# Performance work log

Measured on AMD Instinct MI355X. Metric: run time of the kernel, lower is better.

## Reference

```python
import jax, jax.numpy as jnp
import numpy as np

B, D_IN, D_H = 8192, 512, 1024


def setup_inputs() -> dict:
    key = jax.random.key(0)
    ks = jax.random.split(key, 5)
    # Kaiming-normal-ish init: std = sqrt(2/fan_in)
    Wx = jax.random.normal(ks[0], (D_IN, 4 * D_H), jnp.float32) * np.sqrt(2.0 / D_IN)
    Wh = jax.random.normal(ks[1], (D_H, 4 * D_H), jnp.float32) * np.sqrt(2.0 / D_H)
    b = jnp.zeros((4 * D_H,), jnp.float32)
    x = jax.random.normal(ks[2], (B, D_IN), jnp.float32)
    h = jax.random.normal(ks[3], (B, D_H), jnp.float32)
    c = jax.random.normal(ks[4], (B, D_H), jnp.float32)
    return {"x": x, "h": h, "c": c, "Wx": Wx, "Wh": Wh, "b": b}


def reference(x, h, c, Wx, Wh, b):
    # Fused gate pre-activations: [B, 4H] in gate order (g, i, f, o)
    gates = x @ Wx + h @ Wh + b[None, :]
    g_in, i_in, f_in, o_in = jnp.split(gates, 4, axis=-1)
    g_out = jnp.tanh(g_in)
    i_out = jax.nn.sigmoid(i_in)
    # NOTE: faithful to the original source's bug — f_out and o_out both use i_in.
    f_out = jax.nn.sigmoid(i_in)
    o_out = jax.nn.sigmoid(i_in)
    c_new = g_out * i_out + f_out * c
    h_new = jnp.tanh(c_new) * o_out
    return h_new, c_new
```

## Files before the change

kernel.cpp:

```cpp
#include <hip/hip_runtime.h>
#include <hip/hip_bf16.h>
#include <cstdint>

#define BROWS 8192
#define DIN   512
#define DH    1024
#define KTOT  1536
#define NT    (KTOT / 64)

typedef __bf16 bf16x8 __attribute__((ext_vector_type(8)));
typedef __bf16 bf16x4 __attribute__((ext_vector_type(4)));
typedef float  f32x4  __attribute__((ext_vector_type(4)));

__device__ __forceinline__ void load16_to_lds(const void* gptr, void* lptr) {
    __builtin_amdgcn_global_load_lds(
        (const __attribute__((address_space(1))) uint32_t*)gptr,
        (__attribute__((address_space(3))) uint32_t*)lptr,
        16, 0, 0);
}

__global__ __launch_bounds__(256) void cvtA_kernel(
    const float* __restrict__ x, const float* __restrict__ h,
    __bf16* __restrict__ A) {
    int t = blockIdx.x * 256 + threadIdx.x;
    int row = t / 192;
    int j = t - row * 192;
    int kg = j * 8;
    const float* src = (kg < DIN) ? (x + (size_t)row * DIN + kg)
                                  : (h + (size_t)row * DH + (kg - DIN));
    float4 u = *(const float4*)src;
    float4 v = *(const float4*)(src + 4);
    bf16x8 o = { (__bf16)u.x, (__bf16)u.y, (__bf16)u.z, (__bf16)u.w,
                 (__bf16)v.x, (__bf16)v.y, (__bf16)v.z, (__bf16)v.w };
    int swz = (j * 16) ^ ((row & 7) << 4);
    *(bf16x8*)((char*)A + (size_t)row * 3072 + swz) = o;
}

__global__ __launch_bounds__(256) void cvtB_kernel(
    const float* __restrict__ Wx, const float* __restrict__ Wh,
    __bf16* __restrict__ Bt) {
    __shared__ float tile[32][33];
    int k0 = blockIdx.x * 32;
    int n0 = blockIdx.y * 32;
    int tx = threadIdx.x;
    int ty = threadIdx.y;
#pragma unroll
    for (int i = 0; i < 4; ++i) {
        int k = k0 + ty + 8 * i;
        float v = (k < DIN) ? Wx[(size_t)k * 4096 + n0 + tx]
                            : Wh[(size_t)(k - DIN) * 4096 + n0 + tx];
        tile[ty + 8 * i][tx] = v;
    }
    __syncthreads();
    int n = n0 + tx;
    int kk = ty * 4;
    bf16x4 o = { (__bf16)tile[kk][tx], (__bf16)tile[kk + 1][tx],
                 (__bf16)tile[kk + 2][tx], (__bf16)tile[kk + 3][tx] };
    int swz = ((k0 + kk) * 2) ^ ((n & 7) << 4);
    *(bf16x4*)((char*)Bt + (size_t)n * 3072 + swz) = o;
}


#define BARRIER  do { __builtin_amdgcn_sched_barrier(0); __builtin_amdgcn_s_barrier(); __builtin_amdgcn_sched_barrier(0); } while (0)
#define VMW(n)   do { asm volatile("s_waitcnt vmcnt(" #n ")" ::: "memory"); __builtin_amdgcn_sched_barrier(0); } while (0)
#define LGKM0    do { asm volatile("s_waitcnt lgkmcnt(0)" ::: "memory"); __builtin_amdgcn_sched_barrier(0); } while (0)

#define STAGE_A(buf, kt) do {                                                  \
    const char* g0_ = Ab + (size_t)(brow + r0) * 3072                          \
                         + (size_t)(kt) * 128 + cb;                            \
    char* l0_ = sAb + (buf) * 16384 + r0 * 128 + cb;                           \
    load16_to_lds(g0_, l0_);                                                   \
    load16_to_lds(g0_ + 64 * 3072, l0_ + 64 * 128);                            \
} while (0)

#define STAGE_BG(buf, kt) do {                                                 \
    const char* g0_ = Bb + (size_t)(bnp + r0) * 3072                           \
                         + (size_t)(kt) * 128 + cb;                            \
    load16_to_lds(g0_, sBb + (buf) * 16384 + r0 * 128 + cb);                   \
} while (0)

#define STAGE_BI(buf, kt) do {                                                 \
    const char* g0_ = Bb + (size_t)(1024 + bnp + r0) * 3072                    \
                         + (size_t)(kt) * 128 + cb;                            \
    load16_to_lds(g0_, sBb + (buf) * 16384 + (64 + r0) * 128 + cb);            \
} while (0)

#define READ_A(dst, c)                                                         \
    _Pragma("unroll")                                                          \
    for (int m2_ = 0; m2_ < 2; ++m2_) {                                        \
        _Pragma("unroll")                                                      \
        for (int ks_ = 0; ks_ < 2; ++ks_) {                                    \
            int row_ = wrow + m2_ * 16 + l15;                                  \
            int kb_ = ks_ * 64 + l4x16;                                        \
            dst[m2_][ks_] = *(const bf16x8*)(sAb + (c) * 16384 + row_ * 128    \
                                             + (kb_ ^ swzkey));                \
        }                                                                      \
    }

#define READ_BG(dst, c)                                                        \
    _Pragma("unroll")                                                          \
    for (int ni_ = 0; ni_ < 2; ++ni_) {                                        \
        _Pragma("unroll")                                                      \
        for (int ks_ = 0; ks_ < 2; ++ks_) {                                    \
            int row_ = wcol + ni_ * 16 + l15;                                  \
            int kb_ = ks_ * 64 + l4x16;                                        \
            dst[ni_][ks_] = *(const bf16x8*)(sBb + (c) * 16384 + row_ * 128    \
                                             + (kb_ ^ swzkey));                \
        }                                                                      \
    }

#define READ_BI(dst, c)                                                        \
    _Pragma("unroll")                                                          \
    for (int ni_ = 0; ni_ < 2; ++ni_) {                                        \
        _Pragma("unroll")                                                      \
        for (int ks_ = 0; ks_ < 2; ++ks_) {                                    \
            int row_ = 64 + wcol + ni_ * 16 + l15;                             \
            int kb_ = ks_ * 64 + l4x16;                                        \
            dst[ni_][ks_] = *(const bf16x8*)(sBb + (c) * 16384 + row_ * 128    \
                                             + (kb_ ^ swzkey));                \
        }                                                                      \
    }

#define MMA(ACC, AF, BF) do {                                                  \
    __builtin_amdgcn_s_setprio(1);                                             \
    _Pragma("unroll")                                                          \
    for (int ks_ = 0; ks_ < 2; ++ks_) {                                        \
        _Pragma("unroll")                                                      \
        for (int m2_ = 0; m2_ < 2; ++m2_) {                                    \
            _Pragma("unroll")                                                  \
            for (int ni_ = 0; ni_ < 2; ++ni_) {                                \
                ACC[m2_][ni_] = __builtin_amdgcn_mfma_f32_16x16x32_bf16(       \
                    AF[m2_][ks_], BF[ni_][ks_], ACC[m2_][ni_], 0, 0, 0);       \
            }                                                                  \
        }                                                                      \
    }                                                                          \
    __builtin_amdgcn_s_setprio(0);                                             \
    __builtin_amdgcn_sched_barrier(0);                                         \
} while (0)

__global__ __launch_bounds__(512, 4) void lstm_gemm_kernel(
    const __bf16* __restrict__ A,
    const __bf16* __restrict__ Bt,
    const float* __restrict__ bias,
    const float* __restrict__ c_in,
    float* __restrict__ out_h,
    float* __restrict__ out_c) {
    __shared__ __bf16 sA[2][128][64];
    __shared__ __bf16 sB[2][128][64];

    const int tid  = threadIdx.x;
    const int lane = tid & 63;
    const int wid  = tid >> 6;
    const int wr   = wid & 3;
    const int wc   = wid >> 2;

    const int bid   = blockIdx.x;
    const int xcd   = bid & 7;
    const int idx   = bid >> 3;
    const int band  = xcd * 8 + (idx & 7);
    const int panel = idx >> 3;
    const int brow  = band * 128;
    const int bnp   = panel * 64;

    const int l15    = lane & 15;
    const int l4x16  = (lane >> 4) * 16;
    const int swzkey = (l15 & 7) << 4;
    const int wrow   = wr * 32;
    const int wcol   = wc * 32;

    const int r0 = tid >> 3;
    const int cb = (tid & 7) * 16;

    const char* Ab = (const char*)A;
    const char* Bb = (const char*)Bt;
    char* sAb = (char*)&sA[0][0][0];
    char* sBb = (char*)&sB[0][0][0];

    f32x4 accg[2][2], acci[2][2];
#pragma unroll
    for (int mi = 0; mi < 2; ++mi)
#pragma unroll
        for (int ni = 0; ni < 2; ++ni) {
            accg[mi][ni] = (f32x4){0.f, 0.f, 0.f, 0.f};
            acci[mi][ni] = (f32x4){0.f, 0.f, 0.f, 0.f};
        }

    bf16x8 aF[2][2], bgF[2][2], biF[2][2];

    STAGE_A(0, 0);
    STAGE_BG(0, 0);
    STAGE_BI(0, 0);

    for (int t = 0; t < NT - 1; ++t) {
        const int c  = t & 1;
        const int nb = c ^ 1;
        VMW(1); BARRIER;
        READ_A(aF, c);
        READ_BG(bgF, c);
        STAGE_A(nb, t + 1);
        BARRIER; LGKM0;
        MMA(accg, aF, bgF);
        VMW(2); BARRIER;
        READ_BI(biF, c);
        STAGE_BG(nb, t + 1);
        STAGE_BI(nb, t + 1);
        BARRIER; LGKM0;
        MMA(acci, aF, biF);
    }
    {
        const int c = (NT - 1) & 1;
        VMW(1); BARRIER;
        READ_A(aF, c);
        READ_BG(bgF, c);
        BARRIER; LGKM0;
        MMA(accg, aF, bgF);
        VMW(0); BARRIER;
        READ_BI(biF, c);
        BARRIER; LGKM0;
        MMA(acci, aF, biF);
    }

    const int R0 = brow + wrow;
    const int C0 = bnp + wcol;
    const int l4 = lane >> 4;
#pragma unroll
    for (int ni = 0; ni < 2; ++ni) {
        const int col = C0 + ni * 16 + l15;
        const float bg = bias[col];
        const float bi = bias[1024 + col];
#pragma unroll
        for (int mi = 0; mi < 2; ++mi) {
#pragma unroll
            for (int r = 0; r < 4; ++r) {
                const int row = R0 + mi * 16 + l4 * 4 + r;
                const float g_in = accg[mi][ni][r] + bg;
                const float i_in = acci[mi][ni][r] + bi;
                const float s  = 1.0f / (1.0f + __expf(-i_in));
                const float tg = 2.0f / (1.0f + __expf(-2.0f * g_in)) - 1.0f;
                const float cv = c_in[(size_t)row * DH + col];
                const float cn = s * (tg + cv);
                const float hn = (2.0f / (1.0f + __expf(-2.0f * cn)) - 1.0f) * s;
                out_h[(size_t)row * DH + col] = hn;
                out_c[(size_t)row * DH + col] = cn;
            }
        }
    }
}

extern "C" void kernel_launch(void* const* d_in, const int* in_sizes, int n_in,
                              void* d_out, int out_size, void* d_ws, size_t ws_size,
                              hipStream_t stream) {
    const float* x  = (const float*)d_in[0];
    const float* h  = (const float*)d_in[1];
    const float* c  = (const float*)d_in[2];
    const float* Wx = (const float*)d_in[3];
    const float* Wh = (const float*)d_in[4];
    const float* b  = (const float*)d_in[5];

    __bf16* A  = (__bf16*)d_ws;
    __bf16* Bt = (__bf16*)((char*)d_ws + (size_t)BROWS * KTOT * 2);

    float* out_h = (float*)d_out;
    float* out_c = out_h + (size_t)BROWS * DH;

    cvtA_kernel<<<(BROWS * (KTOT / 8)) / 256, 256, 0, stream>>>(x, h, A);
    cvtB_kernel<<<dim3(KTOT / 32, 2048 / 32), dim3(32, 8), 0, stream>>>(Wx, Wh, Bt);
    lstm_gemm_kernel<<<1024, 512, 0, stream>>>(A, Bt, b, c, out_h, out_c);
}
```

Before: 84.37 us.

## Load B fragments directly from global memory, keeping only A staged in LDS

The weight (B) operand no longer goes through LDS. Each wave reads its B fragments straight from global memory in an unswizzled layout, while only the A tile is double-buffered in shared memory. Blocks shrink to 4 waves, each covering 64 rows, with a new block-to-tile mapping and fewer barriers. This cuts LDS traffic and synchronisation, but exposes global-memory latency on B and leans on L2 reuse of the weights across blocks.

```diff
diff --git a/kernel.cpp b/kernel.cpp
--- a/kernel.cpp
+++ b/kernel.cpp
@@ -56,8 +56,7 @@
     int kk = ty * 4;
     bf16x4 o = { (__bf16)tile[kk][tx], (__bf16)tile[kk + 1][tx],
                  (__bf16)tile[kk + 2][tx], (__bf16)tile[kk + 3][tx] };
-    int swz = ((k0 + kk) * 2) ^ ((n & 7) << 4);
-    *(bf16x4*)((char*)Bt + (size_t)n * 3072 + swz) = o;
+    *(bf16x4*)(Bt + (size_t)n * KTOT + k0 + kk) = o;
 }
 
 
@@ -66,71 +65,50 @@
 #define LGKM0    do { asm volatile("s_waitcnt lgkmcnt(0)" ::: "memory"); __builtin_amdgcn_sched_barrier(0); } while (0)
 
 #define STAGE_A(buf, kt) do {                                                  \
-    const char* g0_ = Ab + (size_t)(brow + r0) * 3072                          \
-                         + (size_t)(kt) * 128 + cb;                            \
-    char* l0_ = sAb + (buf) * 16384 + r0 * 128 + cb;                           \
-    load16_to_lds(g0_, l0_);                                                   \
-    load16_to_lds(g0_ + 64 * 3072, l0_ + 64 * 128);                            \
+    _Pragma("unroll")                                                          \
+    for (int p_ = 0; p_ < 4; ++p_) {                                           \
+        const char* g_ = Ab + (size_t)(brow + p_ * 32 + r0) * 3072             \
+                            + (size_t)(kt) * 128 + cb;                         \
+        load16_to_lds(g_, sAb + (buf) * 16384 + (p_ * 32 + r0) * 128 + cb);    \
+    }                                                                          \
+    __builtin_amdgcn_sched_barrier(0);                                         \
 } while (0)
 
-#define STAGE_BG(buf, kt) do {                                                 \
-    const char* g0_ = Bb + (size_t)(bnp + r0) * 3072                           \
-                         + (size_t)(kt) * 128 + cb;                            \
-    load16_to_lds(g0_, sBb + (buf) * 16384 + r0 * 128 + cb);                   \
-} while (0)
-
-#define STAGE_BI(buf, kt) do {                                                 \
-    const char* g0_ = Bb + (size_t)(1024 + bnp + r0) * 3072                    \
-                         + (size_t)(kt) * 128 + cb;                            \
-    load16_to_lds(g0_, sBb + (buf) * 16384 + (64 + r0) * 128 + cb);            \
-} while (0)
-
-#define READ_A(dst, c)                                                         \
-    _Pragma("unroll")                                                          \
-    for (int m2_ = 0; m2_ < 2; ++m2_) {                                        \
+#define READ_A(c)                                                              \
+    _Pragma("unroll")                                                          \
+    for (int m_ = 0; m_ < 4; ++m_) {                                           \
         _Pragma("unroll")                                                      \
         for (int ks_ = 0; ks_ < 2; ++ks_) {                                    \
-            int row_ = wrow + m2_ * 16 + l15;                                  \
+            int row_ = wrow + m_ * 16 + l15;                                   \
             int kb_ = ks_ * 64 + l4x16;                                        \
-            dst[m2_][ks_] = *(const bf16x8*)(sAb + (c) * 16384 + row_ * 128    \
-                                             + (kb_ ^ swzkey));                \
+            aF[m_][ks_] = *(const bf16x8*)(sAb + (c) * 16384 + row_ * 128      \
+                                           + (kb_ ^ swzkey));                  \
         }                                                                      \
     }
 
-#define READ_BG(dst, c)                                                        \
+#define LOAD_B(dst, rowbase, kt) do {                                          \
     _Pragma("unroll")                                                          \
     for (int ni_ = 0; ni_ < 2; ++ni_) {                                        \
         _Pragma("unroll")                                                      \
         for (int ks_ = 0; ks_ < 2; ++ks_) {                                    \
-            int row_ = wcol + ni_ * 16 + l15;                                  \
-            int kb_ = ks_ * 64 + l4x16;                                        \
-            dst[ni_][ks_] = *(const bf16x8*)(sBb + (c) * 16384 + row_ * 128    \
-                                             + (kb_ ^ swzkey));                \
+            dst[ni_][ks_] = *(const bf16x8*)(Bt                                \
+                + (size_t)((rowbase) + ni_ * 16) * KTOT                        \
+                + (kt) * 64 + ks_ * 32 + l4x8);                                \
         }                                                                      \
-    }
-
-#define READ_BI(dst, c)                                                        \
-    _Pragma("unroll")                                                          \
-    for (int ni_ = 0; ni_ < 2; ++ni_) {                                        \
-        _Pragma("unroll")                                                      \
-        for (int ks_ = 0; ks_ < 2; ++ks_) {                                    \
-            int row_ = 64 + wcol + ni_ * 16 + l15;                             \
-            int kb_ = ks_ * 64 + l4x16;                                        \
-            dst[ni_][ks_] = *(const bf16x8*)(sBb + (c) * 16384 + row_ * 128    \
-                                             + (kb_ ^ swzkey));                \
-        }                                                                      \
-    }
+    }                                                                          \
+    __builtin_amdgcn_sched_barrier(0);                                         \
+} while (0)
 
 #define MMA(ACC, AF, BF) do {                                                  \
     __builtin_amdgcn_s_setprio(1);                                             \
     _Pragma("unroll")                                                          \
     for (int ks_ = 0; ks_ < 2; ++ks_) {                                        \
         _Pragma("unroll")                                                      \
-        for (int m2_ = 0; m2_ < 2; ++m2_) {                                    \
+        for (int m_ = 0; m_ < 4; ++m_) {                                       \
             _Pragma("unroll")                                                  \
             for (int ni_ = 0; ni_ < 2; ++ni_) {                                \
-                ACC[m2_][ni_] = __builtin_amdgcn_mfma_f32_16x16x32_bf16(       \
-                    AF[m2_][ks_], BF[ni_][ks_], ACC[m2_][ni_], 0, 0, 0);       \
+                ACC[m_][ni_] = __builtin_amdgcn_mfma_f32_16x16x32_bf16(        \
+                    AF[m_][ks_], BF[ni_][ks_], ACC[m_][ni_], 0, 0, 0);         \
             }                                                                  \
         }                                                                      \
     }                                                                          \
@@ -138,7 +116,7 @@
     __builtin_amdgcn_sched_barrier(0);                                         \
 } while (0)
 
-__global__ __launch_bounds__(512, 4) void lstm_gemm_kernel(
+__global__ __launch_bounds__(256, 3) void lstm_gemm_kernel(
     const __bf16* __restrict__ A,
     const __bf16* __restrict__ Bt,
     const float* __restrict__ bias,
@@ -146,82 +124,80 @@
     float* __restrict__ out_h,
     float* __restrict__ out_c) {
     __shared__ __bf16 sA[2][128][64];
-    __shared__ __bf16 sB[2][128][64];
 
     const int tid  = threadIdx.x;
     const int lane = tid & 63;
     const int wid  = tid >> 6;
-    const int wr   = wid & 3;
-    const int wc   = wid >> 2;
+    const int wr   = wid & 1;
+    const int wc   = wid >> 1;
 
     const int bid   = blockIdx.x;
-    const int xcd   = bid & 7;
-    const int idx   = bid >> 3;
-    const int band  = xcd * 8 + (idx & 7);
-    const int panel = idx >> 3;
+    const int rg    = bid & 15;
+    const int m     = bid >> 4;
+    const int band  = (rg >> 2) * 16 + (m & 15);
+    const int panel = (rg & 3) * 4 + (m >> 4);
     const int brow  = band * 128;
     const int bnp   = panel * 64;
 
     const int l15    = lane & 15;
     const int l4x16  = (lane >> 4) * 16;
+    const int l4x8   = (lane >> 4) * 8;
     const int swzkey = (l15 & 7) << 4;
-    const int wrow   = wr * 32;
-    const int wcol   = wc * 32;
+    const int wrow   = wr * 64;
 
     const int r0 = tid >> 3;
     const int cb = (tid & 7) * 16;
 
+    const int rowg = bnp + wc * 32 + l15;
+    const int rowi = 1024 + rowg;
+
     const char* Ab = (const char*)A;
-    const char* Bb = (const char*)Bt;
     char* sAb = (char*)&sA[0][0][0];
-    char* sBb = (char*)&sB[0][0][0];
-
-    f32x4 accg[2][2], acci[2][2];
-#pragma unroll
-    for (int mi = 0; mi < 2; ++mi)
+
+    f32x4 accg[4][2], acci[4][2];
+#pragma unroll
+    for (int mi = 0; mi < 4; ++mi)
 #pragma unroll
         for (int ni = 0; ni < 2; ++ni) {
             accg[mi][ni] = (f32x4){0.f, 0.f, 0.f, 0.f};
             acci[mi][ni] = (f32x4){0.f, 0.f, 0.f, 0.f};
         }
 
-    bf16x8 aF[2][2], bgF[2][2], biF[2][2];
+    bf16x8 aF[4][2], bgF[2][2], biF[2][2];
 
     STAGE_A(0, 0);
-    STAGE_BG(0, 0);
-    STAGE_BI(0, 0);
 
     for (int t = 0; t < NT - 1; ++t) {
         const int c  = t & 1;
         const int nb = c ^ 1;
-        VMW(1); BARRIER;
-        READ_A(aF, c);
-        READ_BG(bgF, c);
+        LOAD_B(bgF, rowg, t);
+        LOAD_B(biF, rowi, t);
+        VMW(8);
+        BARRIER;
+        READ_A(c);
         STAGE_A(nb, t + 1);
-        BARRIER; LGKM0;
+        LGKM0;
+        VMW(8);
         MMA(accg, aF, bgF);
-        VMW(2); BARRIER;
-        READ_BI(biF, c);
-        STAGE_BG(nb, t + 1);
-        STAGE_BI(nb, t + 1);
-        BARRIER; LGKM0;
+        VMW(4);
         MMA(acci, aF, biF);
     }
     {
         const int c = (NT - 1) & 1;
-        VMW(1); BARRIER;
-        READ_A(aF, c);
-        READ_BG(bgF, c);
-        BARRIER; LGKM0;
+        LOAD_B(bgF, rowg, NT - 1);
+        LOAD_B(biF, rowi, NT - 1);
+        VMW(8);
+        BARRIER;
+        READ_A(c);
+        LGKM0;
+        VMW(4);
         MMA(accg, aF, bgF);
-        VMW(0); BARRIER;
-        READ_BI(biF, c);
-        BARRIER; LGKM0;
+        VMW(0);
         MMA(acci, aF, biF);
     }
 
     const int R0 = brow + wrow;
-    const int C0 = bnp + wcol;
+    const int C0 = bnp + wc * 32;
     const int l4 = lane >> 4;
 #pragma unroll
     for (int ni = 0; ni < 2; ++ni) {
@@ -229,7 +205,7 @@
         const float bg = bias[col];
         const float bi = bias[1024 + col];
 #pragma unroll
-        for (int mi = 0; mi < 2; ++mi) {
+        for (int mi = 0; mi < 4; ++mi) {
 #pragma unroll
             for (int r = 0; r < 4; ++r) {
                 const int row = R0 + mi * 16 + l4 * 4 + r;
@@ -265,5 +241,5 @@
 
     cvtA_kernel<<<(BROWS * (KTOT / 8)) / 256, 256, 0, stream>>>(x, h, A);
     cvtB_kernel<<<dim3(KTOT / 32, 2048 / 32), dim3(32, 8), 0, stream>>>(Wx, Wh, Bt);
-    lstm_gemm_kernel<<<1024, 512, 0, stream>>>(A, Bt, b, c, out_h, out_c);
-}
+    lstm_gemm_kernel<<<1024, 256, 0, stream>>>(A, Bt, b, c, out_h, out_c);
+}
```

New measurement: 136.0 us. 61.2% more time.
